# Kernel optimization log

Hardware: AMD Instinct MI355X
Metric: run time of the kernel (lower is better)

## Reference

```python
import jax, jax.numpy as jnp
import numpy as np

# Static configuration (from init_kwargs)
B, T, SP = 4, 100, 20          # batch, max_time_patches, max_space_patches
S = T * SP                      # flattened seq len = 2000
H, NH = 512, 8                  # hidden size, heads
D = H // NH                     # head dim = 64
CF, CB = 4, 4                   # context_forward, context_backward
ROPE_BASE = 10000.0
NEG = -1e9


def setup_inputs() -> dict:
    key = jax.random.key(0)
    ks = jax.random.split(key, 8)
    w = 1.0 / np.sqrt(H)
    x = jax.random.normal(ks[0], (B, S, H), jnp.float32)
    # token order is space-major: timestamps = time-patch id repeated per space patch
    timestamps = jnp.broadcast_to(jnp.tile(jnp.arange(T, dtype=jnp.int32), SP), (B, S))
    attn_mask = jnp.ones((B, S), jnp.int32)
    Wq = jax.random.normal(ks[1], (H, H), jnp.float32) * w
    Wk = jax.random.normal(ks[2], (H, H), jnp.float32) * w
    Wv = jax.random.normal(ks[3], (H, H), jnp.float32) * w
    Wo = jax.random.normal(ks[4], (H, H), jnp.float32) * w
    z = jnp.zeros((H,), jnp.float32)
    return {"x": x, "attn_mask": attn_mask, "timestamps": timestamps,
            "Wq": Wq, "bq": z, "Wk": Wk, "bk": z, "Wv": Wv, "bv": z,
            "Wo": Wo, "bo": z}


def _rotate_half(u):
    return jnp.concatenate((-u[..., D // 2:], u[..., :D // 2]), axis=-1)


def _rope_tables():
    inv_freq = 1.0 / (ROPE_BASE ** (jnp.arange(0, D, 2, dtype=jnp.float32) / D))
    t = jnp.arange(T, dtype=jnp.float32)
    freqs = t[:, None] * inv_freq[None, :]          # [T, D/2]
    emb = jnp.concatenate((freqs, freqs), axis=-1)  # [T, D]
    return jnp.cos(emb), jnp.sin(emb)


def _context_mask():
    # forward/backward banded window in time, tiled over space patches
    ones = jnp.ones((T, T), jnp.float32)
    m = jnp.triu(ones, k=-CF).T          # allow up to CF future time patches
    if CB > 0:
        m = m * jnp.triu(ones, k=-CB)    # allow up to CB past time patches
    return jnp.tile(m, (SP, SP))         # [S, S]


def reference(x, attn_mask, timestamps, Wq, bq, Wk, bk, Wv, bv, Wo, bo):
    # projections -> [B, NH, S, D]
    def heads(w, b):
        return (x @ w + b).reshape(B, S, NH, D).transpose(0, 2, 1, 3)
    q, k, v = heads(Wq, bq), heads(Wk, bk), heads(Wv, bv)

    # rotary position embedding indexed by time-patch timestamps
    cos_t, sin_t = _rope_tables()
    cos = cos_t[timestamps][:, None]     # [B, 1, S, D]
    sin = sin_t[timestamps][:, None]
    q = q * cos + _rotate_half(q) * sin
    k = k * cos + _rotate_half(k) * sin

    # banded-context masked attention
    scores = jnp.einsum('bhqd,bhkd->bhqk', q, k) / jnp.sqrt(jnp.float32(D))
    mask = (_context_mask()[None, None, :, :] *
            attn_mask[:, None, None, :].astype(jnp.float32)) > 0
    scores = jnp.where(mask, scores, NEG)
    attn = jax.nn.softmax(scores, axis=-1)
    out = jnp.einsum('bhqk,bhkd->bhqd', attn, v)
    out = out.transpose(0, 2, 1, 3).reshape(B, S, H)
    return out @ Wo + bo
```

## Files before the change

kernel.cpp:

```cpp
#include <hip/hip_runtime.h>
#include <hip/hip_bf16.h>
#include <stdint.h>


typedef __bf16 bf16x8 __attribute__((ext_vector_type(8)));
typedef float f32x4 __attribute__((ext_vector_type(4)));

static const size_t O_XB = 0;
static const size_t O_WT = 8192000;
static const size_t O_Q  = 10289152;
static const size_t O_K  = 18481152;
static const size_t O_V  = 26673152;
static const size_t O_RC = 34865152;
static const size_t O_RS = 34877952;

__device__ inline void gload16(const void* g, void* l) {
  __builtin_amdgcn_global_load_lds((const __attribute__((address_space(1))) void*)g,
                                   (__attribute__((address_space(3))) void*)l, 16, 0, 0);
}

__device__ inline int xcd_swz(int orig, int nwg) {
  const int q8 = nwg >> 3, r8 = nwg & 7;
  const int xcd = orig & 7;
  return (xcd < r8 ? xcd * (q8 + 1) : r8 * (q8 + 1) + (xcd - r8) * q8) + (orig >> 3);
}

__global__ __launch_bounds__(256) void prep_kernel(
    const float* __restrict__ x, const float* __restrict__ Wq, const float* __restrict__ Wk,
    const float* __restrict__ Wv, const float* __restrict__ Wo,
    __bf16* __restrict__ xb, __bf16* __restrict__ wt,
    float* __restrict__ ropeC, float* __restrict__ ropeS)
{
  __shared__ float tile[64][65];
  const int tid = threadIdx.x;
  const int bx = blockIdx.x;
  if (bx < 4000) {
    const int idx = bx * 256 + tid;
    float4 v = ((const float4*)x)[idx];
    union { ushort4 u; __bf16 b[4]; } p;
    p.b[0] = (__bf16)v.x; p.b[1] = (__bf16)v.y; p.b[2] = (__bf16)v.z; p.b[3] = (__bf16)v.w;
    ((ushort4*)xb)[idx] = p.u;
    return;
  }
  const int wb = bx - 4000;
  const int mat = wb >> 6, sub = wb & 63;
  const int tk = (sub >> 3) * 64, tn = (sub & 7) * 64;
  const float* W = (mat == 0) ? Wq : (mat == 1) ? Wk : (mat == 2) ? Wv : Wo;
#pragma unroll
  for (int it = 0; it < 16; ++it) {
    const int idx = it * 256 + tid;
    const int kl = idx >> 6, nl = idx & 63;
    tile[kl][nl] = W[(size_t)(tk + kl) * 512 + tn + nl];
  }
  __syncthreads();
#pragma unroll
  for (int it = 0; it < 16; ++it) {
    const int idx = it * 256 + tid;
    const int nl = idx >> 6, kl = idx & 63;
    wt[(size_t)mat * 262144 + (size_t)(tn + nl) * 512 + tk + kl] = (__bf16)tile[kl][nl];
  }
  if (wb == 0) {
    for (int idx = tid; idx < 3200; idx += 256) {
      const int t = idx >> 5, i = idx & 31;
      const float f = (float)t * powf(10000.0f, -(float)i / 32.0f);
      ropeC[idx] = cosf(f);
      ropeS[idx] = sinf(f);
    }
  }
}

__global__ __launch_bounds__(256) void qkv_fused(
    const __bf16* __restrict__ xb, const __bf16* __restrict__ wt,
    const float* __restrict__ bq, const float* __restrict__ bk, const float* __restrict__ bv,
    const float* __restrict__ ropeC, const float* __restrict__ ropeS,
    __bf16* __restrict__ qws, __bf16* __restrict__ kws, __bf16* __restrict__ vws)
{
  const int tid = threadIdx.x;
  const int wgid = xcd_swz(blockIdx.x, 500);
  const int mt = wgid >> 2, nt = wgid & 3;
  const int m0 = mt * 64, n0 = nt * 128;
  __shared__ __bf16 As[2 * 2048];
  __shared__ __bf16 Bs[2 * 3 * 4096];
  __shared__ int posTbl[64];
  f32x4 acc[3][2][4] = {};
  const int wid = tid >> 6, lane = tid & 63;
  const int wm = (wid >> 1) << 5, wn = (wid & 1) << 6;
  const int lr = lane & 15, g = lane >> 4;

  if (tid < 64) {
    const int m = m0 + tid;
    const int b = m / 2000;
    const int s = m - b * 2000;
    const int t = s % 100;
    const int sp = s / 100;
    posTbl[tid] = ((b * 16000 + t * 20 + sp) << 7) | t;
  }

  const __bf16* a_src = xb + (size_t)(m0 + (tid >> 2)) * 512 + (tid & 3) * 8;

#define STG(BUF, KK) do {                                                        \
    gload16(a_src + (KK), As + (BUF) * 2048 + tid * 8);                          \
    _Pragma("unroll")                                                            \
    for (int mm = 0; mm < 3; ++mm)                                               \
      _Pragma("unroll")                                                          \
      for (int jj = 0; jj < 2; ++jj) {                                           \
        const int c = tid + jj * 256;                                            \
        gload16(wt + (size_t)mm * 262144 + (size_t)(n0 + (c >> 2)) * 512 + (KK)  \
                    + (c & 3) * 8,                                               \
                Bs + ((BUF) * 3 + mm) * 4096 + c * 8);                           \
      }                                                                          \
  } while (0)

  STG(0, 0);
  __syncthreads();

  int cur = 0;
  for (int kks = 0; kks < 16; ++kks) {
    if (kks < 15) STG(cur ^ 1, (kks + 1) * 32);
    bf16x8 af[2];
#pragma unroll
    for (int f = 0; f < 2; ++f)
      af[f] = *(const bf16x8*)(As + cur * 2048 + (wm + f * 16 + lr) * 32 + g * 8);
#pragma unroll
    for (int mat = 0; mat < 3; ++mat) {
      bf16x8 bfr[4];
#pragma unroll
      for (int f = 0; f < 4; ++f)
        bfr[f] = *(const bf16x8*)(Bs + (cur * 3 + mat) * 4096 + (wn + f * 16 + lr) * 32 + g * 8);
#pragma unroll
      for (int i = 0; i < 2; ++i)
#pragma unroll
        for (int j = 0; j < 4; ++j)
          acc[mat][i][j] = __builtin_amdgcn_mfma_f32_16x16x32_bf16(af[i], bfr[j], acc[mat][i][j], 0, 0, 0);
    }
    __syncthreads();
    cur ^= 1;
  }
#undef STG

  const int hn = (n0 + wn) >> 6;
#pragma unroll
  for (int mat = 0; mat < 3; ++mat) {
    const float* bias = (mat == 0) ? bq : (mat == 1) ? bk : bv;
    __bf16* outp = (mat == 0) ? qws : (mat == 1) ? kws : vws;
    const float qscale = (mat == 0) ? 0.125f : 1.0f;
#pragma unroll
    for (int i = 0; i < 2; ++i) {
#pragma unroll
      for (int r = 0; r < 4; ++r) {
        const int row = wm + i * 16 + g * 4 + r;
        const int pk = posTbl[row];
        const int t = pk & 127;
        const size_t ob = ((size_t)((pk >> 7) + hn * 2000)) * 64;
        if (mat == 2) {
#pragma unroll
          for (int j = 0; j < 4; ++j) {
            float v = acc[mat][i][j][r] + bias[n0 + wn + j * 16 + lr];
            outp[ob + j * 16 + lr] = (__bf16)v;
          }
        } else {
#pragma unroll
          for (int j = 0; j < 2; ++j) {
            const int dlo = j * 16 + lr;
            const float alo = acc[mat][i][j][r]     + bias[n0 + wn + j * 16 + lr];
            const float ahi = acc[mat][i][j + 2][r] + bias[n0 + wn + (j + 2) * 16 + lr];
            const float cs = ropeC[t * 32 + dlo], sn = ropeS[t * 32 + dlo];
            const float olo = (alo * cs - ahi * sn) * qscale;
            const float ohi = (ahi * cs + alo * sn) * qscale;
            outp[ob + dlo]      = (__bf16)olo;
            outp[ob + dlo + 32] = (__bf16)ohi;
          }
        }
      }
    }
  }
}

__global__ __launch_bounds__(256) void attn_kernel(
    const __bf16* __restrict__ qw, const __bf16* __restrict__ kw, const __bf16* __restrict__ vw,
    const int* __restrict__ amask, __bf16* __restrict__ aout)
{
  const int wid = threadIdx.x >> 6, lane = threadIdx.x & 63;
  const int tid = threadIdx.x;
  const int lr = lane & 15, g = lane >> 4;
  const int tq = blockIdx.x * 4 + wid;
  const int h = blockIdx.y, b = blockIdx.z;

  int t0 = tq - 4; if (t0 < 0) t0 = 0;
  int t1 = tq + 4; if (t1 > 99) t1 = 99;
  const int k0 = t0 * 20;
  const int nk = (t1 - t0 + 1) * 20;
  const int basew = k0 & ~7;

  const int tq0 = blockIdx.x * 4;
  int t0b = tq0 - 4; if (t0b < 0) t0b = 0;
  int t1b = tq0 + 7; if (t1b > 99) t1b = 99;
  const int kb0 = (t0b * 20) & ~7;
  const int nks = (t1b + 1) * 20 - kb0;
  const int woff = basew - kb0;

  __shared__ __bf16 Vs[64][264];
  __shared__ __bf16 Pl[4][20][200];
  __shared__ float addm[4][192];

  const size_t hb = (size_t)(b * 8 + h) * 2000;
  const __bf16* qp = qw + (hb + (size_t)tq * 20) * 64;
  const __bf16* vp = vw + (hb + (size_t)kb0) * 64;

  for (int k = lane; k < 192; k += 64) {
    const int kg = basew + k;
    float v = -1e9f;
    if (kg >= k0 && kg < k0 + nk) {
      const int tk = kg / 20;
      const int spk = kg - tk * 20;
      if (amask[b * 2000 + spk * 100 + tk] != 0) v = 0.0f;
    }
    addm[wid][k] = v;
  }

  for (int idx = tid; idx < 264 * 16; idx += 256) {
    const int pr = idx >> 4, d4 = (idx & 15) * 4;
    union { ushort4 u; __bf16 e[4]; } p;
    p.u = make_ushort4(0, 0, 0, 0);
    if (pr < nks) p.u = *(const ushort4*)(vp + (size_t)pr * 64 + d4);
    Vs[d4 + 0][pr] = p.e[0];
    Vs[d4 + 1][pr] = p.e[1];
    Vs[d4 + 2][pr] = p.e[2];
    Vs[d4 + 3][pr] = p.e[3];
  }

  bf16x8 qf[2][2];
#pragma unroll
  for (int jq = 0; jq < 2; ++jq) {
    int q = jq * 16 + lr; if (q > 19) q = 19;
#pragma unroll
    for (int ks = 0; ks < 2; ++ks)
      qf[jq][ks] = *(const bf16x8*)(qp + q * 64 + ks * 32 + g * 8);
  }

  f32x4 acc[12][2] = {};
  __builtin_amdgcn_s_setprio(1);
#pragma unroll
  for (int i = 0; i < 12; ++i) {
    int krow = basew + i * 16 + lr; if (krow > 1999) krow = 1999;
    const __bf16* kr = kw + (hb + (size_t)krow) * 64;
    const bf16x8 af0 = *(const bf16x8*)(kr + g * 8);
    const bf16x8 af1 = *(const bf16x8*)(kr + 32 + g * 8);
    acc[i][0] = __builtin_amdgcn_mfma_f32_16x16x32_bf16(af0, qf[0][0], acc[i][0], 0, 0, 0);
    acc[i][0] = __builtin_amdgcn_mfma_f32_16x16x32_bf16(af1, qf[0][1], acc[i][0], 0, 0, 0);
    acc[i][1] = __builtin_amdgcn_mfma_f32_16x16x32_bf16(af0, qf[1][0], acc[i][1], 0, 0, 0);
    acc[i][1] = __builtin_amdgcn_mfma_f32_16x16x32_bf16(af1, qf[1][1], acc[i][1], 0, 0, 0);
  }
  __builtin_amdgcn_s_setprio(0);

  __syncthreads();

#pragma unroll
  for (int jq = 0; jq < 2; ++jq) {
    float mx = -1e30f;
#pragma unroll
    for (int i = 0; i < 12; ++i)
#pragma unroll
      for (int r = 0; r < 4; ++r) {
        acc[i][jq][r] += addm[wid][i * 16 + g * 4 + r];
        mx = fmaxf(mx, acc[i][jq][r]);
      }
    mx = fmaxf(mx, __shfl_xor(mx, 16));
    mx = fmaxf(mx, __shfl_xor(mx, 32));
    float sm = 0.0f;
#pragma unroll
    for (int i = 0; i < 12; ++i)
#pragma unroll
      for (int r = 0; r < 4; ++r) {
        const float p = __expf(acc[i][jq][r] - mx);
        acc[i][jq][r] = p;
        sm += p;
      }
    sm += __shfl_xor(sm, 16);
    sm += __shfl_xor(sm, 32);
    const float rinv = 1.0f / sm;
    const int q = jq * 16 + lr;
    if (q < 20) {
#pragma unroll
      for (int i = 0; i < 12; ++i) {
        union { ushort4 u; __bf16 e[4]; } pk;
        pk.e[0] = (__bf16)(acc[i][jq][0] * rinv);
        pk.e[1] = (__bf16)(acc[i][jq][1] * rinv);
        pk.e[2] = (__bf16)(acc[i][jq][2] * rinv);
        pk.e[3] = (__bf16)(acc[i][jq][3] * rinv);
        *(ushort4*)&Pl[wid][q][i * 16 + g * 4] = pk.u;
      }
    }
  }

  __syncthreads();

  f32x4 acc2[2][4] = {};
  __builtin_amdgcn_s_setprio(1);
#pragma unroll
  for (int kb = 0; kb < 6; ++kb) {
    const int kvloc = woff + kb * 32 + g * 8;
    bf16x8 bfv[4];
#pragma unroll
    for (int j2 = 0; j2 < 4; ++j2)
      bfv[j2] = *(const bf16x8*)&Vs[j2 * 16 + lr][kvloc];
#pragma unroll
    for (int i2 = 0; i2 < 2; ++i2) {
      int qr = i2 * 16 + lr; if (qr > 19) qr = 19;
      const bf16x8 pa = *(const bf16x8*)&Pl[wid][qr][kb * 32 + g * 8];
#pragma unroll
      for (int j2 = 0; j2 < 4; ++j2)
        acc2[i2][j2] = __builtin_amdgcn_mfma_f32_16x16x32_bf16(pa, bfv[j2], acc2[i2][j2], 0, 0, 0);
    }
  }
  __builtin_amdgcn_s_setprio(0);

#pragma unroll
  for (int i2 = 0; i2 < 2; ++i2)
#pragma unroll
    for (int r = 0; r < 4; ++r) {
      const int q = i2 * 16 + g * 4 + r;
      if (q < 20) {
        const size_t ob = ((size_t)b * 2000 + q * 100 + tq) * 512 + h * 64;
#pragma unroll
        for (int j2 = 0; j2 < 4; ++j2)
          aout[ob + j2 * 16 + lr] = (__bf16)acc2[i2][j2][r];
      }
    }
}

__global__ __launch_bounds__(256) void out_gemm(
    const __bf16* __restrict__ ab, const __bf16* __restrict__ wot,
    const float* __restrict__ bo, float* __restrict__ out)
{
  const int tid = threadIdx.x;
  const int wgid = xcd_swz(blockIdx.x, 126);
  const int mt = wgid >> 1, nt = wgid & 1;
  const int m0 = mt * 128, n0 = nt * 256;
  __shared__ __bf16 As[2 * 4096];
  __shared__ __bf16 Bs[2 * 8192];
  f32x4 acc[4][8] = {};
  const int wid = tid >> 6, lane = tid & 63;
  const int wm = (wid >> 1) << 6, wn = (wid & 1) << 7;
  const int lr = lane & 15, g = lane >> 4;

#define STG2(BUF, KK) do {                                                       \
    _Pragma("unroll")                                                            \
    for (int jj = 0; jj < 2; ++jj) {                                             \
      const int c = tid + jj * 256;                                              \
      int row = m0 + (c >> 2); if (row > 7999) row = 7999;                       \
      gload16(ab + (size_t)row * 512 + (KK) + (c & 3) * 8,                       \
              As + (BUF) * 4096 + c * 8);                                        \
    }                                                                            \
    _Pragma("unroll")                                                            \
    for (int jj = 0; jj < 4; ++jj) {                                             \
      const int c = tid + jj * 256;                                              \
      gload16(wot + (size_t)(n0 + (c >> 2)) * 512 + (KK) + (c & 3) * 8,          \
              Bs + (BUF) * 8192 + c * 8);                                        \
    }                                                                            \
  } while (0)

  STG2(0, 0);
  __syncthreads();

  int cur = 0;
  for (int kks = 0; kks < 16; ++kks) {
    if (kks < 15) STG2(cur ^ 1, (kks + 1) * 32);
    bf16x8 af[4];
#pragma unroll
    for (int f = 0; f < 4; ++f)
      af[f] = *(const bf16x8*)(As + cur * 4096 + (wm + f * 16 + lr) * 32 + g * 8);
#pragma unroll
    for (int j = 0; j < 8; ++j) {
      const bf16x8 bfr = *(const bf16x8*)(Bs + cur * 8192 + (wn + j * 16 + lr) * 32 + g * 8);
#pragma unroll
      for (int i = 0; i < 4; ++i)
        acc[i][j] = __builtin_amdgcn_mfma_f32_16x16x32_bf16(af[i], bfr, acc[i][j], 0, 0, 0);
    }
    __syncthreads();
    cur ^= 1;
  }
#undef STG2

#pragma unroll
  for (int i = 0; i < 4; ++i) {
#pragma unroll
    for (int r = 0; r < 4; ++r) {
      const int m = m0 + wm + i * 16 + g * 4 + r;
      if (m < 8000) {
#pragma unroll
        for (int j = 0; j < 8; ++j) {
          const int n = n0 + wn + j * 16 + lr;
          out[(size_t)m * 512 + n] = acc[i][j][r] + bo[n];
        }
      }
    }
  }
}

extern "C" void kernel_launch(void* const* d_in, const int* in_sizes, int n_in,
                              void* d_out, int out_size, void* d_ws, size_t ws_size,
                              hipStream_t stream) {
  const float* x   = (const float*)d_in[0];
  const int* amask = (const int*)d_in[1];
  const float* Wq = (const float*)d_in[3];
  const float* bq = (const float*)d_in[4];
  const float* Wk = (const float*)d_in[5];
  const float* bk = (const float*)d_in[6];
  const float* Wv = (const float*)d_in[7];
  const float* bv = (const float*)d_in[8];
  const float* Wo = (const float*)d_in[9];
  const float* bo = (const float*)d_in[10];
  float* out = (float*)d_out;

  char* ws = (char*)d_ws;
  __bf16* xb    = (__bf16*)(ws + O_XB);
  __bf16* wt    = (__bf16*)(ws + O_WT);
  __bf16* qws   = (__bf16*)(ws + O_Q);
  __bf16* kws   = (__bf16*)(ws + O_K);
  __bf16* vws   = (__bf16*)(ws + O_V);
  float*  ropeC = (float*)(ws + O_RC);
  float*  ropeS = (float*)(ws + O_RS);
  __bf16* aout  = (__bf16*)(ws + O_XB);

  prep_kernel<<<4256, 256, 0, stream>>>(x, Wq, Wk, Wv, Wo, xb, wt, ropeC, ropeS);
  qkv_fused<<<500, 256, 0, stream>>>(xb, wt, bq, bk, bv, ropeC, ropeS, qws, kws, vws);
  attn_kernel<<<dim3(25, 8, 4), 256, 0, stream>>>(qws, kws, vws, amask, aout);
  out_gemm<<<126, 256, 0, stream>>>(aout, wt + 3 * 262144, bo, out);
}
```

Baseline: 98.57 us.

## Retile output GEMM to 64x128 with triple-buffered pipeline and drop attention barrier

The output projection GEMM moves from 126 workgroups of 128x256 tiles to 500 workgroups of 64x128 tiles so more CUs are occupied. It uses a three-stage LDS ring with explicit vmcnt waits instead of double buffering. The attention kernel drops a __syncthreads before the softmax and pads the V shared tile differently to change bank mapping. The removed barrier and odd padding risk races or misaligned vector LDS accesses.

```diff
diff --git a/kernel.cpp b/kernel.cpp
--- a/kernel.cpp
+++ b/kernel.cpp
@@ -199,7 +199,7 @@
   const int nks = (t1b + 1) * 20 - kb0;
   const int woff = basew - kb0;
 
-  __shared__ __bf16 Vs[64][264];
+  __shared__ __bf16 Vs[64][266];
   __shared__ __bf16 Pl[4][20][200];
   __shared__ float addm[4][192];
 
@@ -253,8 +253,6 @@
   }
   __builtin_amdgcn_s_setprio(0);
 
-  __syncthreads();
-
 #pragma unroll
   for (int jq = 0; jq < 2; ++jq) {
     float mx = -1e30f;
@@ -334,65 +332,85 @@
     const float* __restrict__ bo, float* __restrict__ out)
 {
   const int tid = threadIdx.x;
-  const int wgid = xcd_swz(blockIdx.x, 126);
-  const int mt = wgid >> 1, nt = wgid & 1;
-  const int m0 = mt * 128, n0 = nt * 256;
-  __shared__ __bf16 As[2 * 4096];
-  __shared__ __bf16 Bs[2 * 8192];
-  f32x4 acc[4][8] = {};
+  const int wgid = xcd_swz(blockIdx.x, 500);
+  const int mt = wgid >> 2, nt = wgid & 3;
+  const int m0 = mt * 64, n0 = nt * 128;
+  __shared__ __bf16 As[3 * 2048];
+  __shared__ __bf16 Bs[3 * 4096];
+  f32x4 acc[2][4] = {};
   const int wid = tid >> 6, lane = tid & 63;
-  const int wm = (wid >> 1) << 6, wn = (wid & 1) << 7;
+  const int wm = (wid >> 1) << 5, wn = (wid & 1) << 6;
   const int lr = lane & 15, g = lane >> 4;
 
-#define STG2(BUF, KK) do {                                                       \
+  const __bf16* a_src = ab + (size_t)(m0 + (tid >> 2)) * 512 + (tid & 3) * 8;
+
+#define STGO(BUF, KK) do {                                                       \
+    gload16(a_src + (KK), As + (BUF) * 2048 + tid * 8);                          \
     _Pragma("unroll")                                                            \
     for (int jj = 0; jj < 2; ++jj) {                                             \
       const int c = tid + jj * 256;                                              \
-      int row = m0 + (c >> 2); if (row > 7999) row = 7999;                       \
-      gload16(ab + (size_t)row * 512 + (KK) + (c & 3) * 8,                       \
-              As + (BUF) * 4096 + c * 8);                                        \
-    }                                                                            \
-    _Pragma("unroll")                                                            \
-    for (int jj = 0; jj < 4; ++jj) {                                             \
-      const int c = tid + jj * 256;                                              \
       gload16(wot + (size_t)(n0 + (c >> 2)) * 512 + (KK) + (c & 3) * 8,          \
-              Bs + (BUF) * 8192 + c * 8);                                        \
+              Bs + (BUF) * 4096 + c * 8);                                        \
     }                                                                            \
   } while (0)
 
-  STG2(0, 0);
+  STGO(0, 0);
+  STGO(1, 32);
   __syncthreads();
 
-  int cur = 0;
-  for (int kks = 0; kks < 16; ++kks) {
-    if (kks < 15) STG2(cur ^ 1, (kks + 1) * 32);
-    bf16x8 af[4];
+  int cur = 0, st = 2;
+  for (int k = 0; k < 14; ++k) {
+    STGO(st, (k + 2) * 32);
+    {
+      bf16x8 af[2], bfr[4];
+#pragma unroll
+      for (int f = 0; f < 2; ++f)
+        af[f] = *(const bf16x8*)(As + cur * 2048 + (wm + f * 16 + lr) * 32 + g * 8);
+#pragma unroll
+      for (int f = 0; f < 4; ++f)
+        bfr[f] = *(const bf16x8*)(Bs + cur * 4096 + (wn + f * 16 + lr) * 32 + g * 8);
+#pragma unroll
+      for (int i = 0; i < 2; ++i)
+#pragma unroll
+        for (int j = 0; j < 4; ++j)
+          acc[i][j] = __builtin_amdgcn_mfma_f32_16x16x32_bf16(af[i], bfr[j], acc[i][j], 0, 0, 0);
+    }
+    asm volatile("s_waitcnt vmcnt(3)" ::: "memory");
+    __builtin_amdgcn_s_barrier();
+    __builtin_amdgcn_sched_barrier(0);
+    if (++cur == 3) cur = 0;
+    if (++st == 3) st = 0;
+  }
+#pragma unroll
+  for (int tail = 0; tail < 2; ++tail) {
+    const int buf = (tail == 0) ? 2 : 0;
+    if (tail == 0) {
+      asm volatile("s_waitcnt vmcnt(0)" ::: "memory");
+    }
+    bf16x8 af[2], bfr[4];
+#pragma unroll
+    for (int f = 0; f < 2; ++f)
+      af[f] = *(const bf16x8*)(As + buf * 2048 + (wm + f * 16 + lr) * 32 + g * 8);
 #pragma unroll
     for (int f = 0; f < 4; ++f)
-      af[f] = *(const bf16x8*)(As + cur * 4096 + (wm + f * 16 + lr) * 32 + g * 8);
-#pragma unroll
-    for (int j = 0; j < 8; ++j) {
-      const bf16x8 bfr = *(const bf16x8*)(Bs + cur * 8192 + (wn + j * 16 + lr) * 32 + g * 8);
-#pragma unroll
-      for (int i = 0; i < 4; ++i)
-        acc[i][j] = __builtin_amdgcn_mfma_f32_16x16x32_bf16(af[i], bfr, acc[i][j], 0, 0, 0);
-    }
-    __syncthreads();
-    cur ^= 1;
-  }
-#undef STG2
-
-#pragma unroll
-  for (int i = 0; i < 4; ++i) {
+      bfr[f] = *(const bf16x8*)(Bs + buf * 4096 + (wn + f * 16 + lr) * 32 + g * 8);
+#pragma unroll
+    for (int i = 0; i < 2; ++i)
+#pragma unroll
+      for (int j = 0; j < 4; ++j)
+        acc[i][j] = __builtin_amdgcn_mfma_f32_16x16x32_bf16(af[i], bfr[j], acc[i][j], 0, 0, 0);
+  }
+#undef STGO
+
+#pragma unroll
+  for (int i = 0; i < 2; ++i) {
 #pragma unroll
     for (int r = 0; r < 4; ++r) {
       const int m = m0 + wm + i * 16 + g * 4 + r;
-      if (m < 8000) {
-#pragma unroll
-        for (int j = 0; j < 8; ++j) {
-          const int n = n0 + wn + j * 16 + lr;
-          out[(size_t)m * 512 + n] = acc[i][j][r] + bo[n];
-        }
+#pragma unroll
+      for (int j = 0; j < 4; ++j) {
+        const int n = n0 + wn + j * 16 + lr;
+        out[(size_t)m * 512 + n] = acc[i][j][r] + bo[n];
       }
     }
   }
@@ -426,5 +444,5 @@
   prep_kernel<<<4256, 256, 0, stream>>>(x, Wq, Wk, Wv, Wo, xb, wt, ropeC, ropeS);
   qkv_fused<<<500, 256, 0, stream>>>(xb, wt, bq, bk, bv, ropeC, ropeS, qws, kws, vws);
   attn_kernel<<<dim3(25, 8, 4), 256, 0, stream>>>(qws, kws, vws, amask, aout);
-  out_gemm<<<126, 256, 0, stream>>>(aout, wt + 3 * 262144, bo, out);
-}
+  out_gemm<<<500, 256, 0, stream>>>(aout, wt + 3 * 262144, bo, out);
+}
```

New measurement: 85.62 us. -13.1%, faster.
